# Performance work log

Measured on AMD Instinct MI355X. Metric: run time of the kernel, lower is better.

## Reference

```python
import jax, jax.numpy as jnp
import numpy as np

B, T, C = 4, 2048, 1024


def setup_inputs() -> dict:
    key = jax.random.key(0)
    ks = jax.random.split(key, 7)
    s = 1.0 / np.sqrt(C)
    return {
        "x": jax.random.normal(ks[0], (B, T, C), dtype=jnp.float32),
        "Wq": jax.random.normal(ks[1], (C, C), dtype=jnp.float32) * s,
        "bq": jnp.zeros((C,), dtype=jnp.float32),
        "Wk": jax.random.normal(ks[2], (C, C), dtype=jnp.float32) * s,
        "bk": jnp.zeros((C,), dtype=jnp.float32),
        "Wv": jax.random.normal(ks[3], (C, C), dtype=jnp.float32) * s,
        "bv": jnp.zeros((C,), dtype=jnp.float32),
    }


def reference(x, Wq, bq, Wk, bk, Wv, bv):
    # q/k/v projections (torch Linear: x @ W^T + b; here W stored as [C_in, C_out])
    q = x @ Wq + bq  # (B, T, C)
    k = x @ Wk + bk
    v = x @ Wv + bv
    scale = 1.0 / jnp.sqrt(jnp.asarray(C, dtype=x.dtype))
    att = jnp.einsum("btc,bsc->bts", q, k) * scale  # (B, T, T)
    # causal mask: additive -inf above the diagonal
    causal = jnp.tril(jnp.ones((T, T), dtype=bool))
    att = jnp.where(causal, att, jnp.asarray(-jnp.inf, dtype=att.dtype))
    att = jax.nn.softmax(att, axis=-1)
    # dropout is identity in eval/reference mode
    out = jnp.einsum("bts,bsc->btc", att, v)  # (B, T, C)
    return out
```

## Files before the change

kernel.cpp:

```cpp
#include <hip/hip_runtime.h>

#define B_ 4
#define T_ 2048
#define C_ 1024

typedef unsigned short u16;
typedef unsigned int u32;
typedef short sh8 __attribute__((ext_vector_type(8)));
typedef float f32x4 __attribute__((ext_vector_type(4)));

__device__ __forceinline__ float bf2f(u16 u) {
    union { float f; u32 i; } c; c.i = ((u32)u) << 16; return c.f;
}
__device__ __forceinline__ u16 f2bf(float f) {
    union { float f; u32 i; } c; c.f = f;
    return (u16)((c.i + 0x7FFFu + ((c.i >> 16) & 1u)) >> 16);
}

__device__ __forceinline__ void gload_lds16(const void* g, void* l) {
    __builtin_amdgcn_global_load_lds(
        (const __attribute__((address_space(1))) u32*)g,
        (__attribute__((address_space(3))) u32*)l, 16, 0, 0);
}

__device__ __forceinline__ void wait_vm8()   { asm volatile("s_waitcnt vmcnt(8)" ::: "memory"); }
__device__ __forceinline__ void wait_vm0()   { asm volatile("s_waitcnt vmcnt(0)" ::: "memory"); }
__device__ __forceinline__ void barrier_raw(){ asm volatile("s_barrier" ::: "memory"); }

template<bool RS>
__device__ __forceinline__ void mm_core(
    const u16* __restrict__ A, const u16* __restrict__ B,
    int ldA, int ldB, int nk64,
    u16* lds, f32x4 (&acc)[4][4], f32x4* rsacc, int tid)
{
    const int w  = tid >> 6, l = tid & 63;
    const int fr = l & 15,  fq = l >> 4;
    const int wm = (w & 1) << 6, wn = (w >> 1) << 6;
    const int rl = l >> 3;
    const int pc = l & 7;
    const int cg = pc ^ rl;

    sh8 ones;
    if (RS) {
#pragma unroll
        for (int e = 0; e < 8; ++e) ones[e] = (short)0x3F80;
    }

    auto issue = [&](int kt) {
        const int ko = kt << 6;
        u16* dA = lds + ((kt & 1) << 14);
        u16* dB = dA + 8192;
#pragma unroll
        for (int t = 0; t < 4; ++t) {
            const int r0 = w * 32 + t * 8;
            const int r  = r0 + rl;
            gload_lds16(A + (size_t)r * ldA + ko + cg * 8, dA + ((size_t)r0 * 8 + l) * 8);
            gload_lds16(B + (size_t)r * ldB + ko + cg * 8, dB + ((size_t)r0 * 8 + l) * 8);
        }
    };

    issue(0);
    issue(1);

    for (int kt = 0; kt < nk64; ++kt) {
        if (kt + 1 < nk64) wait_vm8(); else wait_vm0();
        barrier_raw();
        u16* bufA = lds + ((kt & 1) << 14);
        u16* bufB = bufA + 8192;
#pragma unroll
        for (int kk = 0; kk < 2; ++kk) {
            sh8 af[4], bf[4];
            const int g = kk * 4 + fq;
#pragma unroll
            for (int i = 0; i < 4; ++i) {
                const int m = wm + i * 16 + fr;
                af[i] = *(const sh8*)(bufA + ((size_t)m * 8 + (g ^ (m & 7))) * 8);
                const int n = wn + i * 16 + fr;
                bf[i] = *(const sh8*)(bufB + ((size_t)n * 8 + (g ^ (n & 7))) * 8);
            }
#pragma unroll
            for (int i = 0; i < 4; ++i) {
#pragma unroll
                for (int j = 0; j < 4; ++j)
                    acc[i][j] = __builtin_amdgcn_mfma_f32_16x16x32_bf16(af[i], bf[j], acc[i][j], 0, 0, 0);
                if (RS)
                    rsacc[i] = __builtin_amdgcn_mfma_f32_16x16x32_bf16(af[i], ones, rsacc[i], 0, 0, 0);
            }
        }
        barrier_raw();
        if (kt + 2 < nk64) issue(kt + 2);
    }
}

__global__ __launch_bounds__(256) void cvt_all(
    const float* __restrict__ x,
    const float* __restrict__ Wq, const float* __restrict__ Wk, const float* __restrict__ Wv,
    u16* __restrict__ xb, u16* __restrict__ wt)
{
    __shared__ float tile[64][68];
    const int bid = blockIdx.x;
    if (bid < 8192) {
        size_t i = ((size_t)bid * 256 + threadIdx.x) * 4;
        float4 f = *(const float4*)(x + i);
        ushort4 o;
        o.x = f2bf(f.x); o.y = f2bf(f.y); o.z = f2bf(f.z); o.w = f2bf(f.w);
        *(ushort4*)(xb + i) = o;
        return;
    }
    const int r = bid - 8192;
    const int z = r >> 8;
    const int rr = r & 255;
    const int n0 = (rr & 15) * 64, k0 = (rr >> 4) * 64;
    const float* W = z == 0 ? Wq : (z == 1 ? Wk : Wv);
    u16* out = wt + (size_t)z * C_ * C_;
    const int tx = threadIdx.x & 15, ty = threadIdx.x >> 4;
#pragma unroll
    for (int rr2 = 0; rr2 < 4; ++rr2) {
        int row = ty + rr2 * 16;
        *(float4*)&tile[row][tx * 4] = *(const float4*)(W + (size_t)(k0 + row) * C_ + n0 + tx * 4);
    }
    __syncthreads();
#pragma unroll
    for (int rr2 = 0; rr2 < 4; ++rr2) {
        int n = ty + rr2 * 16;
        ushort4 o;
        o.x = f2bf(tile[tx * 4 + 0][n]);
        o.y = f2bf(tile[tx * 4 + 1][n]);
        o.z = f2bf(tile[tx * 4 + 2][n]);
        o.w = f2bf(tile[tx * 4 + 3][n]);
        *(ushort4*)(out + (size_t)(n0 + n) * C_ + k0 + tx * 4) = o;
    }
}

__global__ __launch_bounds__(256, 2) void qkv_mfma(
    const u16* __restrict__ xb, const u16* __restrict__ wt,
    const float* __restrict__ bq, const float* __restrict__ bk, const float* __restrict__ bv,
    u16* __restrict__ qo, u16* __restrict__ ko, u16* __restrict__ vto)
{
    __shared__ __align__(16) u16 smem[32768];
    const int z = blockIdx.z;
    const u16* W = wt + (size_t)z * C_ * C_;
    const float* bias = z == 0 ? bq : (z == 1 ? bk : bv);
    const int n0 = blockIdx.x * 128, m0 = blockIdx.y * 128;
    const int tid = threadIdx.x;
    f32x4 acc[4][4];
#pragma unroll
    for (int i = 0; i < 4; ++i)
#pragma unroll
        for (int j = 0; j < 4; ++j) acc[i][j] = 0.0f;

    mm_core<false>(xb + (size_t)m0 * C_, W + (size_t)n0 * C_, C_, C_, C_ / 64, smem, acc, nullptr, tid);

    const int w = tid >> 6, l = tid & 63, fr = l & 15, fq = l >> 4;
    const int wm = (w & 1) << 6, wn = (w >> 1) << 6;
    if (z < 2) {
#pragma unroll
        for (int i = 0; i < 4; ++i)
#pragma unroll
            for (int j = 0; j < 4; ++j) {
                const int ln = wn + j * 16 + fr;
                const float bb = bias[n0 + ln];
#pragma unroll
                for (int r = 0; r < 4; ++r) {
                    const int lm = wm + i * 16 + fq * 4 + r;
                    smem[lm * 136 + ln] = f2bf(acc[i][j][r] + bb);
                }
            }
        __syncthreads();
        u16* out = z == 0 ? qo : ko;
        const int rr = tid >> 4, cc = tid & 15;
#pragma unroll
        for (int p = 0; p < 8; ++p) {
            const int row = p * 16 + rr;
            uint4 val = *(const uint4*)&smem[row * 136 + cc * 8];
            *(uint4*)(out + (size_t)(m0 + row) * C_ + n0 + cc * 8) = val;
        }
    } else {
#pragma unroll
        for (int i = 0; i < 4; ++i)
#pragma unroll
            for (int j = 0; j < 4; ++j) {
                const int ln = wn + j * 16 + fr;
                const float bb = bias[n0 + ln];
#pragma unroll
                for (int r = 0; r < 4; ++r) {
                    const int lm = wm + i * 16 + fq * 4 + r;
                    smem[lm * 129 + ln] = f2bf(acc[i][j][r] + bb);
                }
            }
        __syncthreads();
        const int b = m0 >> 11;
        const int t0 = m0 & 2047;
        u16* vt = vto + (size_t)b * C_ * T_;
#pragma unroll
        for (int pass = 0; pass < 8; ++pass) {
            const int ln = (tid >> 4) + pass * 16;
            const int c  = tid & 15;
            u16 tmp[8];
#pragma unroll
            for (int e = 0; e < 8; ++e) tmp[e] = smem[(c * 8 + e) * 129 + ln];
            *(uint4*)(vt + (size_t)(n0 + ln) * T_ + t0 + c * 8) = *(uint4*)tmp;
        }
    }
}

__device__ __constant__ size_t att_off[4] = {
    0, (size_t)1 << 22, (size_t)1 << 25, ((size_t)1 << 25) + ((size_t)1 << 22)
};

__global__ __launch_bounds__(256, 2) void scores_mfma(
    const u16* __restrict__ qb, const u16* __restrict__ kb, u16* __restrict__ wsbase)
{
    int t = blockIdx.x;
    int by = (int)((sqrtf(8.f * t + 1.f) - 1.f) * 0.5f);
    while ((by + 1) * (by + 2) / 2 <= t) ++by;
    while (by * (by + 1) / 2 > t) --by;
    const int bx = t - by * (by + 1) / 2;
    const int b = blockIdx.z;
    const int s0 = bx * 128, m0 = by * 128;
    __shared__ __align__(16) u16 smem[32768];
    const u16* Q = qb + (size_t)b * T_ * C_ + (size_t)m0 * C_;
    const u16* K = kb + (size_t)b * T_ * C_ + (size_t)s0 * C_;
    const int tid = threadIdx.x;
    f32x4 acc[4][4];
#pragma unroll
    for (int i = 0; i < 4; ++i)
#pragma unroll
        for (int j = 0; j < 4; ++j) acc[i][j] = 0.0f;

    mm_core<false>(Q, K, C_, C_, C_ / 64, smem, acc, nullptr, tid);

    const int w = tid >> 6, l = tid & 63, fr = l & 15, fq = l >> 4;
    const int wm = (w & 1) << 6, wn = (w >> 1) << 6;
#pragma unroll
    for (int i = 0; i < 4; ++i)
#pragma unroll
        for (int r = 0; r < 4; ++r) {
            const int lm = wm + i * 16 + fq * 4 + r;
            const int m = m0 + lm;
#pragma unroll
            for (int j = 0; j < 4; ++j) {
                const int ls = wn + j * 16 + fr;
                const int s = s0 + ls;
                float e = (s <= m) ? __expf(acc[i][j][r] * 0.03125f) : 0.f;
                smem[lm * 136 + ls] = f2bf(e);
            }
        }
    __syncthreads();
    u16* att = wsbase + att_off[b] + (size_t)m0 * T_ + s0;
    const int rr = tid >> 4, cc = tid & 15;
#pragma unroll
    for (int p = 0; p < 8; ++p) {
        const int row = p * 16 + rr;
        uint4 val = *(const uint4*)&smem[row * 136 + cc * 8];
        *(uint4*)(att + (size_t)row * T_ + cc * 8) = val;
    }
}

__global__ __launch_bounds__(256, 2) void pv_mfma(
    const u16* __restrict__ wsbase, const u16* __restrict__ vt,
    float* __restrict__ outp)
{
    const int b = blockIdx.z;
    const int n0 = blockIdx.x * 128;
    const int by = 15 - blockIdx.y;
    const int m0 = by * 128;
    __shared__ __align__(16) u16 smem[32768];
    const u16* A  = wsbase + att_off[b] + (size_t)m0 * T_;
    const u16* Bp = vt + (size_t)b * C_ * T_ + (size_t)n0 * T_;
    const int tid = threadIdx.x;
    f32x4 acc[4][4], rs[4];
#pragma unroll
    for (int i = 0; i < 4; ++i) {
        rs[i] = 0.0f;
#pragma unroll
        for (int j = 0; j < 4; ++j) acc[i][j] = 0.0f;
    }

    mm_core<true>(A, Bp, T_, T_, (m0 + 128) >> 6, smem, acc, rs, tid);

    const int w = tid >> 6, l = tid & 63, fr = l & 15, fq = l >> 4;
    const int wm = (w & 1) << 6, wn = (w >> 1) << 6;
    float* fb = (float*)smem;
#pragma unroll
    for (int p = 0; p < 2; ++p) {
        if ((w & 1) == p) {
#pragma unroll
            for (int i = 0; i < 4; ++i)
#pragma unroll
                for (int r = 0; r < 4; ++r) {
                    const int rr2 = i * 16 + fq * 4 + r;
                    const float inv = 1.0f / rs[i][r];
#pragma unroll
                    for (int j = 0; j < 4; ++j)
                        fb[rr2 * 132 + wn + j * 16 + fr] = acc[i][j][r] * inv;
                }
        }
        __syncthreads();
        const int rr = tid >> 5, cc = (tid & 31) * 4;
#pragma unroll
        for (int k2 = 0; k2 < 8; ++k2) {
            const int row = k2 * 8 + rr;
            float4 val = *(const float4*)&fb[row * 132 + cc];
            *(float4*)(outp + ((size_t)b * T_ + m0 + p * 64 + row) * C_ + n0 + cc) = val;
        }
        __syncthreads();
    }
}

extern "C" void kernel_launch(void* const* d_in, const int* in_sizes, int n_in,
                              void* d_out, int out_size, void* d_ws, size_t ws_size,
                              hipStream_t stream) {
    const float* x  = (const float*)d_in[0];
    const float* Wq = (const float*)d_in[1];
    const float* bq = (const float*)d_in[2];
    const float* Wk = (const float*)d_in[3];
    const float* bk = (const float*)d_in[4];
    const float* Wv = (const float*)d_in[5];
    const float* bv = (const float*)d_in[6];
    float* out = (float*)d_out;

    char* ws = (char*)d_ws;
    u16* xb   = (u16*)ws;
    u16* q    = (u16*)(ws + (16ull << 20));
    u16* k    = (u16*)(ws + (32ull << 20));
    u16* vt   = (u16*)(ws + (48ull << 20));
    u16* wt   = (u16*)(ws + (64ull << 20));
    u16* attb = (u16*)ws;

    cvt_all <<<8960, 256, 0, stream>>>(x, Wq, Wk, Wv, xb, wt);
    qkv_mfma<<<dim3(8, 64, 3), 256, 0, stream>>>(xb, wt, bq, bk, bv, q, k, vt);
    scores_mfma<<<dim3(136, 1, 4), 256, 0, stream>>>(q, k, attb);
    pv_mfma    <<<dim3(8, 16, 4), 256, 0, stream>>>(attb, vt, out);
}
```

Measured before the change: 243.9 us.

## Rewrite QKV projection as 256x256-tile 8-wave GEMM with 4-stage LDS pipeline

Replaces the 128x128-tile QKV projection kernel with a 512-thread kernel that computes 256x256 output tiles. It uses a 4-deep buffered global-to-LDS pipeline over K-slices of 32, with interleaved A/B staging and setprio around the MFMA bursts, plus an XCD-aware block index remap. The goals are more data reuse per LDS load, fewer blocks to schedule, and better overlap of loads with MFMA. The costs are a larger LDS footprint (128KB), which limits occupancy, more accumulator registers per thread, and a swizzled epilogue for the Q/K stores and the V transpose.

```diff
diff --git a/kernel.cpp b/kernel.cpp
--- a/kernel.cpp
+++ b/kernel.cpp
@@ -24,6 +24,7 @@
 }
 
 __device__ __forceinline__ void wait_vm8()   { asm volatile("s_waitcnt vmcnt(8)" ::: "memory"); }
+__device__ __forceinline__ void wait_vm4()   { asm volatile("s_waitcnt vmcnt(4)" ::: "memory"); }
 __device__ __forceinline__ void wait_vm0()   { asm volatile("s_waitcnt vmcnt(0)" ::: "memory"); }
 __device__ __forceinline__ void barrier_raw(){ asm volatile("s_barrier" ::: "memory"); }
 
@@ -132,74 +133,146 @@
     }
 }
 
-__global__ __launch_bounds__(256, 2) void qkv_mfma(
+__global__ __launch_bounds__(512, 2) void qkv8(
     const u16* __restrict__ xb, const u16* __restrict__ wt,
     const float* __restrict__ bq, const float* __restrict__ bk, const float* __restrict__ bv,
     u16* __restrict__ qo, u16* __restrict__ ko, u16* __restrict__ vto)
 {
-    __shared__ __align__(16) u16 smem[32768];
-    const int z = blockIdx.z;
-    const u16* W = wt + (size_t)z * C_ * C_;
+    __shared__ __align__(16) u16 smem[65536];
+    const int bid = blockIdx.x;
+    const int wg  = (bid & 7) * 48 + (bid >> 3);
+    const int z   = wg >> 7;
+    const int tt  = wg & 127;
+    const int n0  = (tt >> 5) << 8;
+    const int m0  = (tt & 31) << 8;
+    const int tid = threadIdx.x;
+
+    const u16* Ag = xb + (size_t)m0 * C_;
+    const u16* Bg = wt + (size_t)z * C_ * C_ + (size_t)n0 * C_;
+
+    const int l  = tid & 63, w = tid >> 6;
+    const int fr = l & 15,  fq = l >> 4;
+    const int wm = (w >> 2) << 7;
+    const int wn = (w & 3) << 6;
+
+    const int srow = tid >> 2, spg = tid & 3;
+    const int slg  = spg ^ ((srow >> 1) & 3);
+    const u16* aS0 = Ag + (size_t)srow * C_ + slg * 8;
+    const u16* aS1 = Ag + (size_t)(srow + 128) * C_ + slg * 8;
+    const u16* bS0 = Bg + (size_t)srow * C_ + slg * 8;
+    const u16* bS1 = Bg + (size_t)(srow + 128) * C_ + slg * 8;
+
+    auto stageA = [&](int sl) {
+        u16* d = smem + ((sl & 3) << 14);
+        gload_lds16(aS0 + sl * 32, d + tid * 8);
+        gload_lds16(aS1 + sl * 32, d + 4096 + tid * 8);
+    };
+    auto stageB = [&](int sl) {
+        u16* d = smem + ((sl & 3) << 14) + 8192;
+        gload_lds16(bS0 + sl * 32, d + tid * 8);
+        gload_lds16(bS1 + sl * 32, d + 4096 + tid * 8);
+    };
+
+    f32x4 acc[8][4];
+#pragma unroll
+    for (int i = 0; i < 8; ++i)
+#pragma unroll
+        for (int j = 0; j < 4; ++j) acc[i][j] = 0.0f;
+
+    stageA(0); stageB(0);
+    stageA(1); stageB(1);
+    stageA(2); stageB(2);
+    wait_vm8();
+    barrier_raw();
+
+#pragma unroll 4
+    for (int sk = 0; sk < 32; ++sk) {
+        const u16* bA = smem + ((sk & 3) << 14);
+        const u16* bB = bA + 8192;
+        sh8 af[8], bf[2];
+#pragma unroll
+        for (int i = 0; i < 8; ++i) {
+            const int m = wm + i * 16 + fr;
+            af[i] = *(const sh8*)(bA + ((m << 2) + (fq ^ ((m >> 1) & 3))) * 8);
+        }
+#pragma unroll
+        for (int jj = 0; jj < 2; ++jj) {
+            const int n = wn + jj * 16 + fr;
+            bf[jj] = *(const sh8*)(bB + ((n << 2) + (fq ^ ((n >> 1) & 3))) * 8);
+        }
+        if (sk + 3 < 32) stageA(sk + 3);
+        barrier_raw();
+        __builtin_amdgcn_s_setprio(1);
+#pragma unroll
+        for (int i = 0; i < 8; ++i) {
+            acc[i][0] = __builtin_amdgcn_mfma_f32_16x16x32_bf16(af[i], bf[0], acc[i][0], 0, 0, 0);
+            acc[i][1] = __builtin_amdgcn_mfma_f32_16x16x32_bf16(af[i], bf[1], acc[i][1], 0, 0, 0);
+        }
+        __builtin_amdgcn_s_setprio(0);
+        barrier_raw();
+#pragma unroll
+        for (int jj = 0; jj < 2; ++jj) {
+            const int n = wn + (2 + jj) * 16 + fr;
+            bf[jj] = *(const sh8*)(bB + ((n << 2) + (fq ^ ((n >> 1) & 3))) * 8);
+        }
+        if (sk + 3 < 32) stageB(sk + 3);
+        barrier_raw();
+        __builtin_amdgcn_s_setprio(1);
+#pragma unroll
+        for (int i = 0; i < 8; ++i) {
+            acc[i][2] = __builtin_amdgcn_mfma_f32_16x16x32_bf16(af[i], bf[0], acc[i][2], 0, 0, 0);
+            acc[i][3] = __builtin_amdgcn_mfma_f32_16x16x32_bf16(af[i], bf[1], acc[i][3], 0, 0, 0);
+        }
+        __builtin_amdgcn_s_setprio(0);
+        if      (sk + 3 < 32) wait_vm8();
+        else if (sk + 2 < 32) wait_vm4();
+        else if (sk + 1 < 32) wait_vm0();
+        barrier_raw();
+    }
+
     const float* bias = z == 0 ? bq : (z == 1 ? bk : bv);
-    const int n0 = blockIdx.x * 128, m0 = blockIdx.y * 128;
-    const int tid = threadIdx.x;
-    f32x4 acc[4][4];
-#pragma unroll
-    for (int i = 0; i < 4; ++i)
-#pragma unroll
-        for (int j = 0; j < 4; ++j) acc[i][j] = 0.0f;
-
-    mm_core<false>(xb + (size_t)m0 * C_, W + (size_t)n0 * C_, C_, C_, C_ / 64, smem, acc, nullptr, tid);
-
-    const int w = tid >> 6, l = tid & 63, fr = l & 15, fq = l >> 4;
-    const int wm = (w & 1) << 6, wn = (w >> 1) << 6;
+#pragma unroll
+    for (int j = 0; j < 4; ++j) {
+        const int col = wn + j * 16 + fr;
+        const float bb = bias[n0 + col];
+        const int cg = col >> 3, ce = col & 7;
+#pragma unroll
+        for (int i = 0; i < 8; ++i)
+#pragma unroll
+            for (int r = 0; r < 4; ++r) {
+                const int row = wm + i * 16 + fq * 4 + r;
+                smem[row * 256 + ((cg ^ ((row >> 3) & 31)) << 3) + ce] = f2bf(acc[i][j][r] + bb);
+            }
+    }
+    __syncthreads();
+
     if (z < 2) {
-#pragma unroll
-        for (int i = 0; i < 4; ++i)
-#pragma unroll
-            for (int j = 0; j < 4; ++j) {
-                const int ln = wn + j * 16 + fr;
-                const float bb = bias[n0 + ln];
-#pragma unroll
-                for (int r = 0; r < 4; ++r) {
-                    const int lm = wm + i * 16 + fq * 4 + r;
-                    smem[lm * 136 + ln] = f2bf(acc[i][j][r] + bb);
-                }
-            }
-        __syncthreads();
         u16* out = z == 0 ? qo : ko;
-        const int rr = tid >> 4, cc = tid & 15;
-#pragma unroll
-        for (int p = 0; p < 8; ++p) {
-            const int row = p * 16 + rr;
-            uint4 val = *(const uint4*)&smem[row * 136 + cc * 8];
-            *(uint4*)(out + (size_t)(m0 + row) * C_ + n0 + cc * 8) = val;
+#pragma unroll
+        for (int p = 0; p < 16; ++p) {
+            const int idx = p * 512 + tid;
+            const int row = idx >> 5;
+            const int c16 = idx & 31;
+            uint4 v = *(const uint4*)&smem[row * 256 + ((c16 ^ ((row >> 3) & 31)) << 3)];
+            *(uint4*)(out + (size_t)(m0 + row) * C_ + n0 + c16 * 8) = v;
         }
     } else {
-#pragma unroll
-        for (int i = 0; i < 4; ++i)
-#pragma unroll
-            for (int j = 0; j < 4; ++j) {
-                const int ln = wn + j * 16 + fr;
-                const float bb = bias[n0 + ln];
-#pragma unroll
-                for (int r = 0; r < 4; ++r) {
-                    const int lm = wm + i * 16 + fq * 4 + r;
-                    smem[lm * 129 + ln] = f2bf(acc[i][j][r] + bb);
-                }
-            }
-        __syncthreads();
-        const int b = m0 >> 11;
+        const int b  = m0 >> 11;
         const int t0 = m0 & 2047;
         u16* vt = vto + (size_t)b * C_ * T_;
 #pragma unroll
-        for (int pass = 0; pass < 8; ++pass) {
-            const int ln = (tid >> 4) + pass * 16;
-            const int c  = tid & 15;
+        for (int p = 0; p < 16; ++p) {
+            const int idx = p * 512 + tid;
+            const int cl = idx >> 5;
+            const int ch = idx & 31;
+            const int cg = cl >> 3, ce = cl & 7;
             u16 tmp[8];
 #pragma unroll
-            for (int e = 0; e < 8; ++e) tmp[e] = smem[(c * 8 + e) * 129 + ln];
-            *(uint4*)(vt + (size_t)(n0 + ln) * T_ + t0 + c * 8) = *(uint4*)tmp;
+            for (int e = 0; e < 8; ++e) {
+                const int row = ch * 8 + e;
+                tmp[e] = smem[row * 256 + ((cg ^ ((row >> 3) & 31)) << 3) + ce];
+            }
+            *(uint4*)(vt + (size_t)(n0 + cl) * T_ + t0 + ch * 8) = *(uint4*)tmp;
         }
     }
 }
@@ -329,7 +402,7 @@
     u16* attb = (u16*)ws;
 
     cvt_all <<<8960, 256, 0, stream>>>(x, Wq, Wk, Wv, xb, wt);
-    qkv_mfma<<<dim3(8, 64, 3), 256, 0, stream>>>(xb, wt, bq, bk, bv, q, k, vt);
+    qkv8    <<<384, 512, 0, stream>>>(xb, wt, bq, bk, bv, q, k, vt);
     scores_mfma<<<dim3(136, 1, 4), 256, 0, stream>>>(q, k, attb);
     pv_mfma    <<<dim3(8, 16, 4), 256, 0, stream>>>(attb, vt, out);
 }
```

After: 248.1 us. About the same (+1.7%).

## Use K=32 double-buffered GEMM core to shrink LDS and raise occupancy

Applied to the files above, without the earlier changes.

Adds a new GEMM mainloop that stages 32-wide K slices instead of 64, using a smaller swizzled double buffer. The scores kernel's LDS drops to about 35KB and its launch bound rises to 4 blocks per CU, while the PV kernel uses the same core. MFMA issue is wrapped in s_setprio so math waves get priority. The cost is twice as many barriers and waitcnt iterations per unit of K, and the higher occupancy target may put pressure on registers.

```diff
diff --git a/kernel.cpp b/kernel.cpp
--- a/kernel.cpp
+++ b/kernel.cpp
@@ -24,6 +24,7 @@
 }
 
 __device__ __forceinline__ void wait_vm8()   { asm volatile("s_waitcnt vmcnt(8)" ::: "memory"); }
+__device__ __forceinline__ void wait_vm4()   { asm volatile("s_waitcnt vmcnt(4)" ::: "memory"); }
 __device__ __forceinline__ void wait_vm0()   { asm volatile("s_waitcnt vmcnt(0)" ::: "memory"); }
 __device__ __forceinline__ void barrier_raw(){ asm volatile("s_barrier" ::: "memory"); }
 
@@ -89,6 +90,72 @@
         }
         barrier_raw();
         if (kt + 2 < nk64) issue(kt + 2);
+    }
+}
+
+template<bool RS>
+__device__ __forceinline__ void mm1_core(
+    const u16* __restrict__ A, const u16* __restrict__ B,
+    int ldA, int ldB, int nk32,
+    u16* lds, f32x4 (&acc)[4][4], f32x4* rsacc, int tid)
+{
+    const int w  = tid >> 6, l = tid & 63;
+    const int fr = l & 15,  fq = l >> 4;
+    const int wm = (w & 1) << 6, wn = (w >> 1) << 6;
+
+    sh8 ones;
+    if (RS) {
+#pragma unroll
+        for (int e = 0; e < 8; ++e) ones[e] = (short)0x3F80;
+    }
+
+    const int srow = tid >> 2, spg = tid & 3;
+    const int lg   = spg ^ ((srow >> 1) & 3);
+    const u16* aS0 = A + (size_t)srow * ldA + lg * 8;
+    const u16* aS1 = A + (size_t)(srow + 64) * ldA + lg * 8;
+    const u16* bS0 = B + (size_t)srow * ldB + lg * 8;
+    const u16* bS1 = B + (size_t)(srow + 64) * ldB + lg * 8;
+
+    auto issue = [&](int sk) {
+        u16* d = lds + ((sk & 1) << 13);
+        const int ko = sk << 5;
+        gload_lds16(aS0 + ko, d + (size_t)tid * 8);
+        gload_lds16(aS1 + ko, d + 2048 + (size_t)tid * 8);
+        gload_lds16(bS0 + ko, d + 4096 + (size_t)tid * 8);
+        gload_lds16(bS1 + ko, d + 6144 + (size_t)tid * 8);
+    };
+
+    issue(0);
+    if (nk32 > 1) issue(1);
+
+    for (int sk = 0; sk < nk32; ++sk) {
+        if (sk + 1 < nk32) wait_vm4(); else wait_vm0();
+        barrier_raw();
+        const u16* sA = lds + ((sk & 1) << 13);
+        const u16* sB = sA + 4096;
+        sh8 af[4], bf[4];
+#pragma unroll
+        for (int i = 0; i < 4; ++i) {
+            const int m = wm + i * 16 + fr;
+            af[i] = *(const sh8*)(sA + ((m << 2) + (fq ^ ((m >> 1) & 3))) * 8);
+        }
+#pragma unroll
+        for (int j = 0; j < 4; ++j) {
+            const int n = wn + j * 16 + fr;
+            bf[j] = *(const sh8*)(sB + ((n << 2) + (fq ^ ((n >> 1) & 3))) * 8);
+        }
+        __builtin_amdgcn_s_setprio(1);
+#pragma unroll
+        for (int i = 0; i < 4; ++i) {
+#pragma unroll
+            for (int j = 0; j < 4; ++j)
+                acc[i][j] = __builtin_amdgcn_mfma_f32_16x16x32_bf16(af[i], bf[j], acc[i][j], 0, 0, 0);
+            if (RS)
+                rsacc[i] = __builtin_amdgcn_mfma_f32_16x16x32_bf16(af[i], ones, rsacc[i], 0, 0, 0);
+        }
+        __builtin_amdgcn_s_setprio(0);
+        barrier_raw();
+        if (sk + 2 < nk32) issue(sk + 2);
     }
 }
 
@@ -208,7 +275,7 @@
     0, (size_t)1 << 22, (size_t)1 << 25, ((size_t)1 << 25) + ((size_t)1 << 22)
 };
 
-__global__ __launch_bounds__(256, 2) void scores_mfma(
+__global__ __launch_bounds__(256, 4) void scores_mfma(
     const u16* __restrict__ qb, const u16* __restrict__ kb, u16* __restrict__ wsbase)
 {
     int t = blockIdx.x;
@@ -218,7 +285,7 @@
     const int bx = t - by * (by + 1) / 2;
     const int b = blockIdx.z;
     const int s0 = bx * 128, m0 = by * 128;
-    __shared__ __align__(16) u16 smem[32768];
+    __shared__ __align__(16) u16 smem[17536];
     const u16* Q = qb + (size_t)b * T_ * C_ + (size_t)m0 * C_;
     const u16* K = kb + (size_t)b * T_ * C_ + (size_t)s0 * C_;
     const int tid = threadIdx.x;
@@ -228,10 +295,11 @@
 #pragma unroll
         for (int j = 0; j < 4; ++j) acc[i][j] = 0.0f;
 
-    mm_core<false>(Q, K, C_, C_, C_ / 64, smem, acc, nullptr, tid);
+    mm1_core<false>(Q, K, C_, C_, C_ / 32, smem, acc, nullptr, tid);
 
     const int w = tid >> 6, l = tid & 63, fr = l & 15, fq = l >> 4;
     const int wm = (w & 1) << 6, wn = (w >> 1) << 6;
+    __syncthreads();
 #pragma unroll
     for (int i = 0; i < 4; ++i)
 #pragma unroll
@@ -265,7 +333,7 @@
     const int n0 = blockIdx.x * 128;
     const int by = 15 - blockIdx.y;
     const int m0 = by * 128;
-    __shared__ __align__(16) u16 smem[32768];
+    __shared__ __align__(16) u16 smem[33536];
     const u16* A  = wsbase + att_off[b] + (size_t)m0 * T_;
     const u16* Bp = vt + (size_t)b * C_ * T_ + (size_t)n0 * T_;
     const int tid = threadIdx.x;
@@ -277,11 +345,12 @@
         for (int j = 0; j < 4; ++j) acc[i][j] = 0.0f;
     }
 
-    mm_core<true>(A, Bp, T_, T_, (m0 + 128) >> 6, smem, acc, rs, tid);
+    mm1_core<true>(A, Bp, T_, T_, (m0 + 128) >> 5, smem, acc, rs, tid);
 
     const int w = tid >> 6, l = tid & 63, fr = l & 15, fq = l >> 4;
     const int wm = (w & 1) << 6, wn = (w >> 1) << 6;
     float* fb = (float*)smem;
+    __syncthreads();
 #pragma unroll
     for (int p = 0; p < 2; ++p) {
         if ((w & 1) == p) {
```

Result: no change. 247.8 us (+1.6%).
